# Optimization experiments

Measured on AMD Instinct MI355X. Metric: run time of the kernel, lower is better.

## Reference

```python
import jax, jax.numpy as jnp
import numpy as np

FEATURES = 1024
NUM_HEADS = 16
HEAD_SIZE = FEATURES // NUM_HEADS
B, T = 4, 2048
LN_EPS = 1e-6


def setup_inputs() -> dict:
    key = jax.random.key(0)
    ks = jax.random.split(key, 12)
    C, H, D = FEATURES, NUM_HEADS, HEAD_SIZE
    s_in = 1.0 / np.sqrt(C)
    s_ff = 1.0 / np.sqrt(4 * C)
    return {
        "x": jax.random.normal(ks[0], (B, T, C), jnp.float32),
        # per-head Q/K/V projections (no bias), stacked over heads
        "wq": jax.random.normal(ks[1], (H, C, D), jnp.float32) * s_in,
        "wk": jax.random.normal(ks[2], (H, C, D), jnp.float32) * s_in,
        "wv": jax.random.normal(ks[3], (H, C, D), jnp.float32) * s_in,
        "w_proj": jax.random.normal(ks[4], (C, C), jnp.float32) * s_in,
        "b_proj": jnp.zeros((C,), jnp.float32),
        "w_ff1": jax.random.normal(ks[5], (C, 4 * C), jnp.float32) * s_in,
        "b_ff1": jnp.zeros((4 * C,), jnp.float32),
        "w_ff2": jax.random.normal(ks[6], (4 * C, C), jnp.float32) * s_ff,
        "b_ff2": jnp.zeros((C,), jnp.float32),
        "ln1_scale": jnp.ones((C,), jnp.float32),
        "ln1_bias": jnp.zeros((C,), jnp.float32),
        "ln2_scale": jnp.ones((C,), jnp.float32),
        "ln2_bias": jnp.zeros((C,), jnp.float32),
    }


def _layernorm(x, scale, bias):
    mu = jnp.mean(x, axis=-1, keepdims=True)
    var = jnp.mean(jnp.square(x - mu), axis=-1, keepdims=True)
    return (x - mu) * jax.lax.rsqrt(var + LN_EPS) * scale + bias


def reference(x, wq, wk, wv, w_proj, b_proj, w_ff1, b_ff1, w_ff2, b_ff2,
              ln1_scale, ln1_bias, ln2_scale, ln2_bias):
    Bn, Tn, C = x.shape
    res = x
    xn = _layernorm(x, ln1_scale, ln1_bias)
    # per-head projections, vectorized over heads: [B,H,T,D]
    q = jnp.einsum('btc,hcd->bhtd', xn, wq)
    k = jnp.einsum('btc,hcd->bhtd', xn, wk)
    v = jnp.einsum('btc,hcd->bhtd', xn, wv)
    wei = jnp.einsum('bhtd,bhsd->bhts', q, k)
    tril = jnp.tril(jnp.ones((Tn, Tn), jnp.float32))
    # NOTE: original scales by C**-0.5 (full feature dim, not head_size),
    # and multiplies after masking (-inf * scale stays -inf).
    wei = jnp.where(tril == 0, -jnp.inf, wei) * (C ** -0.5)
    wei = jax.nn.softmax(wei, axis=-1)
    out = jnp.einsum('bhts,bhsd->bhtd', wei, v)
    # concat heads back to [B,T,C]
    out = out.transpose(0, 2, 1, 3).reshape(Bn, Tn, C)
    x = res + out @ w_proj + b_proj
    res = x
    xn = _layernorm(x, ln2_scale, ln2_bias)
    h = jax.nn.relu(xn @ w_ff1 + b_ff1)
    out = res + h @ w_ff2 + b_ff2
    return out
```

## Files before the change

### kernel.cpp

```cpp
#include <hip/hip_runtime.h>

#define Bn 4
#define Tn 2048
#define Cn 1024
#define Hn 16
#define Dn 64
#define Mr (Bn*Tn)

typedef _Float16 half8 __attribute__((ext_vector_type(8)));
typedef _Float16 half4v __attribute__((ext_vector_type(4)));
typedef float f32x4 __attribute__((ext_vector_type(4)));
typedef unsigned u32x4 __attribute__((ext_vector_type(4)));

__device__ __forceinline__ void g2l16(const void* g, void* l) {
  __builtin_amdgcn_global_load_lds((__attribute__((address_space(1))) void*)g,
                                   (__attribute__((address_space(3))) void*)l, 16, 0, 0);
}

__global__ __launch_bounds__(256) void transpose_f32_f16(const float* __restrict__ in,
                                                         _Float16* __restrict__ out,
                                                         int R, int C) {
  __shared__ float tile[32][33];
  const size_t zoff = (size_t)blockIdx.z * R * C;
  in += zoff; out += zoff;
  const int c0 = blockIdx.x * 32, r0 = blockIdx.y * 32;
  const int tx = threadIdx.x, ty = threadIdx.y;
#pragma unroll
  for (int i = 0; i < 4; ++i)
    tile[ty + i*8][tx] = in[(size_t)(r0 + ty + i*8) * C + c0 + tx];
  __syncthreads();
#pragma unroll
  for (int i = 0; i < 4; ++i)
    out[(size_t)(c0 + ty + i*8) * R + r0 + tx] = (_Float16)tile[tx][ty + i*8];
}

__global__ __launch_bounds__(256) void ln_row(const float* __restrict__ x,
                                              const float* __restrict__ g,
                                              const float* __restrict__ bta,
                                              _Float16* __restrict__ out) {
  const int row = blockIdx.x;
  const float4 v = ((const float4*)(x + (size_t)row * Cn))[threadIdx.x];
  float s  = v.x + v.y + v.z + v.w;
  float ss = v.x*v.x + v.y*v.y + v.z*v.z + v.w*v.w;
#pragma unroll
  for (int m = 1; m < 64; m <<= 1) { s += __shfl_xor(s, m); ss += __shfl_xor(ss, m); }
  __shared__ float red[8];
  const int wave = threadIdx.x >> 6, lane = threadIdx.x & 63;
  if (lane == 0) { red[wave] = s; red[4 + wave] = ss; }
  __syncthreads();
  s  = red[0] + red[1] + red[2] + red[3];
  ss = red[4] + red[5] + red[6] + red[7];
  const float mean = s * (1.0f/Cn);
  const float var  = ss * (1.0f/Cn) - mean*mean;
  const float rstd = rsqrtf(var + 1e-6f);
  const int c = threadIdx.x * 4;
  const float4 gg = ((const float4*)g)[threadIdx.x];
  const float4 bb = ((const float4*)bta)[threadIdx.x];
  half4v o;
  o[0] = (_Float16)((v.x - mean) * rstd * gg.x + bb.x);
  o[1] = (_Float16)((v.y - mean) * rstd * gg.y + bb.y);
  o[2] = (_Float16)((v.z - mean) * rstd * gg.z + bb.z);
  o[3] = (_Float16)((v.w - mean) * rstd * gg.w + bb.w);
  *((half4v*)(out + (size_t)row * Cn + c)) = o;
}

enum { EPI_QK = 0, EPI_V = 1, EPI_PROJ = 2, EPI_FF1 = 3, EPI_FF2 = 4 };

template<int EPI>
__global__ __launch_bounds__(256) void gemm_bt(const _Float16* __restrict__ A,
                                               const _Float16* __restrict__ Bt,
                                               void* __restrict__ outp,
                                               const float* __restrict__ bias,
                                               const float* __restrict__ resid,
                                               int M, int N, int K) {
  __shared__ __align__(16) _Float16 As[128*64];
  __shared__ __align__(16) _Float16 Bs[128*64];
  const int tid = threadIdx.x, wave = tid >> 6, lane = tid & 63;
  const int lr = lane & 15, lg = lane >> 4;
  const int brow = blockIdx.y * 128, bcol = blockIdx.x * 128;
  const int wrow = (wave >> 1) * 64, wcol = (wave & 1) * 64;
  f32x4 acc[4][4] = {};

  for (int kt = 0; kt < K; kt += 64) {
#pragma unroll
    for (int i = 0; i < 4; ++i) {
      const int chunk = i*4 + wave;
      const int e = chunk*512 + lane*8;
      const int rr = e >> 6, cc = e & 63;
      g2l16(A  + (size_t)(brow + rr)*K + kt + cc, As + chunk*512);
      g2l16(Bt + (size_t)(bcol + rr)*K + kt + cc, Bs + chunk*512);
    }
    __syncthreads();
#pragma unroll
    for (int kk = 0; kk < 64; kk += 32) {
      half8 af[4], bfr[4];
#pragma unroll
      for (int i = 0; i < 4; ++i) af[i]  = *(const half8*)(As + (wrow + i*16 + lr)*64 + kk + lg*8);
#pragma unroll
      for (int j = 0; j < 4; ++j) bfr[j] = *(const half8*)(Bs + (wcol + j*16 + lr)*64 + kk + lg*8);
#pragma unroll
      for (int i = 0; i < 4; ++i)
#pragma unroll
        for (int j = 0; j < 4; ++j)
          acc[i][j] = __builtin_amdgcn_mfma_f32_16x16x32_f16(af[i], bfr[j], acc[i][j], 0, 0, 0);
    }
    __syncthreads();
  }

  const int r0 = brow + wrow + lg*4;
  const int c0 = bcol + wcol + lr;
#pragma unroll
  for (int i = 0; i < 4; ++i) {
#pragma unroll
    for (int j = 0; j < 4; ++j) {
      const int col = c0 + j*16;
#pragma unroll
      for (int r = 0; r < 4; ++r) {
        const int row = r0 + i*16 + r;
        const float v = acc[i][j][r];
        if constexpr (EPI == EPI_QK) {
          ((_Float16*)outp)[(((size_t)(row >> 11) * Hn + (col >> 6)) * Tn + (row & 2047)) * Dn + (col & 63)] = (_Float16)v;
        } else if constexpr (EPI == EPI_V) {
          ((_Float16*)outp)[(((size_t)(row >> 11) * Hn + (col >> 6)) * Dn + (col & 63)) * Tn + (row & 2047)] = (_Float16)v;
        } else if constexpr (EPI == EPI_PROJ || EPI == EPI_FF2) {
          ((float*)outp)[(size_t)row * N + col] = v + bias[col] + resid[(size_t)row * N + col];
        } else if constexpr (EPI == EPI_FF1) {
          const float t = v + bias[col];
          ((_Float16*)outp)[(size_t)row * N + col] = (_Float16)(t > 0.f ? t : 0.f);
        }
      }
    }
  }
}

__global__ __launch_bounds__(256) void attn_kernel(const _Float16* __restrict__ q,
                                                   const _Float16* __restrict__ k,
                                                   const _Float16* __restrict__ vt,
                                                   _Float16* __restrict__ out) {
  const int qt = (int)(gridDim.x - 1 - blockIdx.x) * 128;
  const int h = blockIdx.y, b = blockIdx.z;
  const int tid = threadIdx.x, wave = tid >> 6, lane = tid & 63;
  const int lr = lane & 15, lg = lane >> 4;
  const size_t bh = (size_t)b * Hn + h;
  const _Float16* qg = q  + bh * (Tn * Dn);
  const _Float16* kg = k  + bh * (Tn * Dn);
  const _Float16* vg = vt + bh * (Dn * Tn);

  __shared__ __align__(16) _Float16 Ks[2][64*64];
  __shared__ __align__(16) _Float16 Vs[2][64*64];

  half8 qf[2][2];
#pragma unroll
  for (int qi = 0; qi < 2; ++qi)
#pragma unroll
    for (int dh = 0; dh < 2; ++dh)
      qf[qi][dh] = *(const half8*)(qg + (size_t)(qt + wave*32 + qi*16 + lr)*Dn + dh*32 + lg*8);

  f32x4 oacc[2][4] = {};
  float mrow[2] = {-__builtin_inff(), -__builtin_inff()};
  float lsum[2] = {0.f, 0.f};

  const int qmax = qt + wave*32 + 31;
  const int nt = (qt + 128) >> 6;

  auto STAGE = [&](int bufi, int t) {
    const int kvt = t * 64;
#pragma unroll
    for (int r = 0; r < 2; ++r) {
      const int g0 = r*256 + wave*64;
      const int g  = g0 + lane;
      const int rr = g >> 3;
      const int cs = (g & 7) ^ (rr & 7);
      g2l16(kg + (size_t)(kvt + rr)*Dn + cs*8, &Ks[bufi][g0*8]);
      g2l16(vg + (size_t)rr*Tn + kvt + cs*8,   &Vs[bufi][g0*8]);
    }
  };

  STAGE(0, 0);
  __syncthreads();

  for (int t = 0; t < nt; ++t) {
    const int kvt = t * 64;
    if (t + 1 < nt) STAGE((t + 1) & 1, t + 1);

    if (kvt <= qmax) {
      const _Float16* KS = Ks[t & 1];
      const _Float16* VS = Vs[t & 1];
      half8 kb[4][2];
#pragma unroll
      for (int f = 0; f < 4; ++f)
#pragma unroll
        for (int dh = 0; dh < 2; ++dh)
          kb[f][dh] = *(const half8*)(KS + (16*f + lr)*64 + (((4*dh + lg) ^ (lr & 7)) * 8));

#pragma unroll
      for (int qi = 0; qi < 2; ++qi) {
        f32x4 sv[4];
#pragma unroll
        for (int f = 0; f < 4; ++f) {
          f32x4 tacc = {0.f, 0.f, 0.f, 0.f};
          tacc = __builtin_amdgcn_mfma_f32_16x16x32_f16(kb[f][0], qf[qi][0], tacc, 0, 0, 0);
          tacc = __builtin_amdgcn_mfma_f32_16x16x32_f16(kb[f][1], qf[qi][1], tacc, 0, 0, 0);
          sv[f] = tacc;
        }
        const int qrow = qt + wave*32 + qi*16 + lr;
#pragma unroll
        for (int f = 0; f < 4; ++f)
#pragma unroll
          for (int r = 0; r < 4; ++r) {
            const int kvv = kvt + 16*f + 4*lg + r;
            sv[f][r] = (kvv > qrow) ? -__builtin_inff() : sv[f][r] * 0.03125f;
          }
        float tm = sv[0][0];
#pragma unroll
        for (int f = 0; f < 4; ++f)
#pragma unroll
          for (int r = 0; r < 4; ++r) tm = fmaxf(tm, sv[f][r]);
        tm = fmaxf(tm, __shfl_xor(tm, 16));
        tm = fmaxf(tm, __shfl_xor(tm, 32));
        const float mn = fmaxf(mrow[qi], tm);
        const float alpha = __expf(mrow[qi] - mn);
        mrow[qi] = mn;
        float ps = 0.f;
#pragma unroll
        for (int f = 0; f < 4; ++f)
#pragma unroll
          for (int r = 0; r < 4; ++r) {
            const float e = __expf(sv[f][r] - mn);
            ps += e;
            sv[f][r] = e;
          }
        ps += __shfl_xor(ps, 16);
        ps += __shfl_xor(ps, 32);
        lsum[qi] = lsum[qi] * alpha + ps;
        unsigned ph[4][2];
#pragma unroll
        for (int f = 0; f < 4; ++f)
#pragma unroll
          for (int m = 0; m < 2; ++m) {
            const unsigned lo = (unsigned)__builtin_bit_cast(unsigned short, (_Float16)sv[f][2*m]);
            const unsigned hi = (unsigned)__builtin_bit_cast(unsigned short, (_Float16)sv[f][2*m + 1]);
            ph[f][m] = lo | (hi << 16);
          }
        float ab[4];
#pragma unroll
        for (int r = 0; r < 4; ++r) ab[r] = __shfl(alpha, 4*lg + r);
#pragma unroll
        for (int df = 0; df < 4; ++df)
#pragma unroll
          for (int r = 0; r < 4; ++r) oacc[qi][df][r] *= ab[r];
        const int s0 = lr + 16*(2*(lg & 1));
        const int s1 = s0 + 16;
        half8 pa[2];
#pragma unroll
        for (int kh = 0; kh < 2; ++kh) {
          u32x4 w = {0u, 0u, 0u, 0u};
#pragma unroll
          for (int fi = 0; fi < 2; ++fi) {
            const unsigned a0 = __shfl(ph[2*kh + fi][0], s0);
            const unsigned a1 = __shfl(ph[2*kh + fi][1], s0);
            const unsigned a2 = __shfl(ph[2*kh + fi][0], s1);
            const unsigned a3 = __shfl(ph[2*kh + fi][1], s1);
            const bool sel = ((lg >> 1) == fi);
            w[0] = sel ? a0 : w[0];
            w[1] = sel ? a1 : w[1];
            w[2] = sel ? a2 : w[2];
            w[3] = sel ? a3 : w[3];
          }
          pa[kh] = __builtin_bit_cast(half8, w);
        }
#pragma unroll
        for (int df = 0; df < 4; ++df) {
          half8 vb0 = *(const half8*)(VS + (16*df + lr)*64 + (((0 + lg) ^ (lr & 7)) * 8));
          half8 vb1 = *(const half8*)(VS + (16*df + lr)*64 + (((4 + lg) ^ (lr & 7)) * 8));
          oacc[qi][df] = __builtin_amdgcn_mfma_f32_16x16x32_f16(pa[0], vb0, oacc[qi][df], 0, 0, 0);
          oacc[qi][df] = __builtin_amdgcn_mfma_f32_16x16x32_f16(pa[1], vb1, oacc[qi][df], 0, 0, 0);
        }
      }
    }
    __syncthreads();
  }

#pragma unroll
  for (int qi = 0; qi < 2; ++qi) {
    const float linv = 1.0f / lsum[qi];
    float lb[4];
#pragma unroll
    for (int r = 0; r < 4; ++r) lb[r] = __shfl(linv, 4*lg + r);
#pragma unroll
    for (int df = 0; df < 4; ++df)
#pragma unroll
      for (int r = 0; r < 4; ++r) {
        const int row = qt + wave*32 + qi*16 + 4*lg + r;
        const int col = h*Dn + df*16 + lr;
        out[((size_t)b*Tn + row)*Cn + col] = (_Float16)(oacc[qi][df][r] * lb[r]);
      }
  }
}

extern "C" void kernel_launch(void* const* d_in, const int* in_sizes, int n_in,
                              void* d_out, int out_size, void* d_ws, size_t ws_size,
                              hipStream_t stream) {
  const float* x      = (const float*)d_in[0];
  const float* wq     = (const float*)d_in[1];
  const float* wk     = (const float*)d_in[2];
  const float* wv     = (const float*)d_in[3];
  const float* w_proj = (const float*)d_in[4];
  const float* b_proj = (const float*)d_in[5];
  const float* b_ff1  = (const float*)d_in[7];
  const float* w_ff1  = (const float*)d_in[6];
  const float* w_ff2  = (const float*)d_in[8];
  const float* b_ff2  = (const float*)d_in[9];
  const float* ln1s   = (const float*)d_in[10];
  const float* ln1b   = (const float*)d_in[11];
  const float* ln2s   = (const float*)d_in[12];
  const float* ln2b   = (const float*)d_in[13];
  float* outp = (float*)d_out;

  char* ws = (char*)d_ws;
  constexpr size_t MB = (size_t)1 << 20;
  _Float16* Wq_t  = (_Float16*)(ws + 0*MB);
  _Float16* Wk_t  = (_Float16*)(ws + 2*MB);
  _Float16* Wv_t  = (_Float16*)(ws + 4*MB);
  _Float16* Wp_t  = (_Float16*)(ws + 6*MB);
  _Float16* Wf1_t = (_Float16*)(ws + 8*MB);
  _Float16* Wf2_t = (_Float16*)(ws + 16*MB);
  _Float16* xn    = (_Float16*)(ws + 24*MB);
  _Float16* attn_o= (_Float16*)(ws + 24*MB);
  _Float16* qbuf  = (_Float16*)(ws + 40*MB);
  _Float16* kbuf  = (_Float16*)(ws + 56*MB);
  _Float16* vtbuf = (_Float16*)(ws + 72*MB);
  _Float16* hbuf  = (_Float16*)(ws + 40*MB);
  float*    x2    = (float*)   (ws + 104*MB);
  _Float16* xn2   = (_Float16*)(ws + 136*MB);

  dim3 tb(32, 8);
  transpose_f32_f16<<<dim3(2, 32, 16), tb, 0, stream>>>(wq, Wq_t, 1024, 64);
  transpose_f32_f16<<<dim3(2, 32, 16), tb, 0, stream>>>(wk, Wk_t, 1024, 64);
  transpose_f32_f16<<<dim3(2, 32, 16), tb, 0, stream>>>(wv, Wv_t, 1024, 64);
  transpose_f32_f16<<<dim3(32, 32, 1), tb, 0, stream>>>(w_proj, Wp_t, 1024, 1024);
  transpose_f32_f16<<<dim3(128, 32, 1), tb, 0, stream>>>(w_ff1, Wf1_t, 1024, 4096);
  transpose_f32_f16<<<dim3(32, 128, 1), tb, 0, stream>>>(w_ff2, Wf2_t, 4096, 1024);

  ln_row<<<Mr, 256, 0, stream>>>(x, ln1s, ln1b, xn);

  gemm_bt<EPI_QK><<<dim3(8, 64), 256, 0, stream>>>(xn, Wq_t, qbuf, nullptr, nullptr, Mr, Cn, Cn);
  gemm_bt<EPI_QK><<<dim3(8, 64), 256, 0, stream>>>(xn, Wk_t, kbuf, nullptr, nullptr, Mr, Cn, Cn);
  gemm_bt<EPI_V ><<<dim3(8, 64), 256, 0, stream>>>(xn, Wv_t, vtbuf, nullptr, nullptr, Mr, Cn, Cn);

  attn_kernel<<<dim3(Tn/128, Hn, Bn), 256, 0, stream>>>(qbuf, kbuf, vtbuf, attn_o);

  gemm_bt<EPI_PROJ><<<dim3(8, 64), 256, 0, stream>>>(attn_o, Wp_t, x2, b_proj, x, Mr, Cn, Cn);

  ln_row<<<Mr, 256, 0, stream>>>(x2, ln2s, ln2b, xn2);

  gemm_bt<EPI_FF1><<<dim3(32, 64), 256, 0, stream>>>(xn2, Wf1_t, hbuf, b_ff1, nullptr, Mr, 4*Cn, Cn);
  gemm_bt<EPI_FF2><<<dim3(8, 64), 256, 0, stream>>>(hbuf, Wf2_t, outp, b_ff2, x2, Mr, Cn, 4*Cn);
}
```

Before: 663.6 us.

## Pair causal query tiles per block to balance attention work and share K/V staging

Each attention block now handles two 128-row query tiles, pi and 15-pi, so every block does about the same amount of causal work. The K/V tiles staged in shared memory are reused by both query tiles. The grid along the sequence axis is halved to 8. The softmax scale is folded into Q in fp16 before the loop, which removes a per-score multiply but adds a small rounding change and doubles accumulator register use, which may lower occupancy.

```diff
diff --git a/kernel.cpp b/kernel.cpp
--- a/kernel.cpp
+++ b/kernel.cpp
@@ -137,7 +137,9 @@
                                                    const _Float16* __restrict__ k,
                                                    const _Float16* __restrict__ vt,
                                                    _Float16* __restrict__ out) {
-  const int qt = (int)(gridDim.x - 1 - blockIdx.x) * 128;
+  const int pi = blockIdx.x;
+  const int qtA = pi * 128;
+  const int qtB = (15 - pi) * 128;
   const int h = blockIdx.y, b = blockIdx.z;
   const int tid = threadIdx.x, wave = tid >> 6, lane = tid & 63;
   const int lr = lane & 15, lg = lane >> 4;
@@ -149,19 +151,25 @@
   __shared__ __align__(16) _Float16 Ks[2][64*64];
   __shared__ __align__(16) _Float16 Vs[2][64*64];
 
-  half8 qf[2][2];
+  const _Float16 qsc = (_Float16)0.03125f;
+  half8 qfA[2][2], qfB[2][2];
 #pragma unroll
   for (int qi = 0; qi < 2; ++qi)
 #pragma unroll
-    for (int dh = 0; dh < 2; ++dh)
-      qf[qi][dh] = *(const half8*)(qg + (size_t)(qt + wave*32 + qi*16 + lr)*Dn + dh*32 + lg*8);
-
-  f32x4 oacc[2][4] = {};
-  float mrow[2] = {-__builtin_inff(), -__builtin_inff()};
-  float lsum[2] = {0.f, 0.f};
-
-  const int qmax = qt + wave*32 + 31;
-  const int nt = (qt + 128) >> 6;
+    for (int dh = 0; dh < 2; ++dh) {
+      half8 a = *(const half8*)(qg + (size_t)(qtA + wave*32 + qi*16 + lr)*Dn + dh*32 + lg*8);
+      half8 c = *(const half8*)(qg + (size_t)(qtB + wave*32 + qi*16 + lr)*Dn + dh*32 + lg*8);
+#pragma unroll
+      for (int j = 0; j < 8; ++j) { a[j] *= qsc; c[j] *= qsc; }
+      qfA[qi][dh] = a; qfB[qi][dh] = c;
+    }
+
+  f32x4 oaccA[2][4] = {}, oaccB[2][4] = {};
+  float mrowA[2] = {-__builtin_inff(), -__builtin_inff()};
+  float mrowB[2] = {-__builtin_inff(), -__builtin_inff()};
+  float lsumA[2] = {0.f, 0.f}, lsumB[2] = {0.f, 0.f};
+
+  const int ntB = (qtB >> 6) + 2;
 
   auto STAGE = [&](int bufi, int t) {
     const int kvt = t * 64;
@@ -176,126 +184,134 @@
     }
   };
 
+  auto COMPUTE = [&](const half8 (&qf)[2][2], f32x4 (&oacc)[2][4],
+                     float* mrow, float* lsum, int qb,
+                     const _Float16* KS, const _Float16* VS, int kvt) {
+    half8 kb[4][2];
+#pragma unroll
+    for (int f = 0; f < 4; ++f)
+#pragma unroll
+      for (int dh = 0; dh < 2; ++dh)
+        kb[f][dh] = *(const half8*)(KS + (16*f + lr)*64 + (((4*dh + lg) ^ (lr & 7)) * 8));
+
+#pragma unroll
+    for (int qi = 0; qi < 2; ++qi) {
+      f32x4 sv[4];
+#pragma unroll
+      for (int f = 0; f < 4; ++f) {
+        f32x4 tacc = {0.f, 0.f, 0.f, 0.f};
+        tacc = __builtin_amdgcn_mfma_f32_16x16x32_f16(kb[f][0], qf[qi][0], tacc, 0, 0, 0);
+        tacc = __builtin_amdgcn_mfma_f32_16x16x32_f16(kb[f][1], qf[qi][1], tacc, 0, 0, 0);
+        sv[f] = tacc;
+      }
+      const int qrow = qb + wave*32 + qi*16 + lr;
+#pragma unroll
+      for (int f = 0; f < 4; ++f)
+#pragma unroll
+        for (int r = 0; r < 4; ++r) {
+          const int kvv = kvt + 16*f + 4*lg + r;
+          sv[f][r] = (kvv > qrow) ? -__builtin_inff() : sv[f][r];
+        }
+      float tm = sv[0][0];
+#pragma unroll
+      for (int f = 0; f < 4; ++f)
+#pragma unroll
+        for (int r = 0; r < 4; ++r) tm = fmaxf(tm, sv[f][r]);
+      tm = fmaxf(tm, __shfl_xor(tm, 16));
+      tm = fmaxf(tm, __shfl_xor(tm, 32));
+      const float mn = fmaxf(mrow[qi], tm);
+      const float alpha = __expf(mrow[qi] - mn);
+      mrow[qi] = mn;
+      float ps = 0.f;
+#pragma unroll
+      for (int f = 0; f < 4; ++f)
+#pragma unroll
+        for (int r = 0; r < 4; ++r) {
+          const float e = __expf(sv[f][r] - mn);
+          ps += e;
+          sv[f][r] = e;
+        }
+      ps += __shfl_xor(ps, 16);
+      ps += __shfl_xor(ps, 32);
+      lsum[qi] = lsum[qi] * alpha + ps;
+      unsigned ph[4][2];
+#pragma unroll
+      for (int f = 0; f < 4; ++f)
+#pragma unroll
+        for (int m = 0; m < 2; ++m) {
+          const unsigned lo = (unsigned)__builtin_bit_cast(unsigned short, (_Float16)sv[f][2*m]);
+          const unsigned hi = (unsigned)__builtin_bit_cast(unsigned short, (_Float16)sv[f][2*m + 1]);
+          ph[f][m] = lo | (hi << 16);
+        }
+      float ab[4];
+#pragma unroll
+      for (int r = 0; r < 4; ++r) ab[r] = __shfl(alpha, 4*lg + r);
+#pragma unroll
+      for (int df = 0; df < 4; ++df)
+#pragma unroll
+        for (int r = 0; r < 4; ++r) oacc[qi][df][r] *= ab[r];
+      const int s0 = lr + 16*(2*(lg & 1));
+      const int s1 = s0 + 16;
+      half8 pa[2];
+#pragma unroll
+      for (int kh = 0; kh < 2; ++kh) {
+        u32x4 w = {0u, 0u, 0u, 0u};
+#pragma unroll
+        for (int fi = 0; fi < 2; ++fi) {
+          const unsigned a0 = __shfl(ph[2*kh + fi][0], s0);
+          const unsigned a1 = __shfl(ph[2*kh + fi][1], s0);
+          const unsigned a2 = __shfl(ph[2*kh + fi][0], s1);
+          const unsigned a3 = __shfl(ph[2*kh + fi][1], s1);
+          const bool sel = ((lg >> 1) == fi);
+          w[0] = sel ? a0 : w[0];
+          w[1] = sel ? a1 : w[1];
+          w[2] = sel ? a2 : w[2];
+          w[3] = sel ? a3 : w[3];
+        }
+        pa[kh] = __builtin_bit_cast(half8, w);
+      }
+#pragma unroll
+      for (int df = 0; df < 4; ++df) {
+        half8 vb0 = *(const half8*)(VS + (16*df + lr)*64 + (((0 + lg) ^ (lr & 7)) * 8));
+        half8 vb1 = *(const half8*)(VS + (16*df + lr)*64 + (((4 + lg) ^ (lr & 7)) * 8));
+        oacc[qi][df] = __builtin_amdgcn_mfma_f32_16x16x32_f16(pa[0], vb0, oacc[qi][df], 0, 0, 0);
+        oacc[qi][df] = __builtin_amdgcn_mfma_f32_16x16x32_f16(pa[1], vb1, oacc[qi][df], 0, 0, 0);
+      }
+    }
+  };
+
   STAGE(0, 0);
   __syncthreads();
 
-  for (int t = 0; t < nt; ++t) {
+  for (int t = 0; t < ntB; ++t) {
     const int kvt = t * 64;
-    if (t + 1 < nt) STAGE((t + 1) & 1, t + 1);
-
-    if (kvt <= qmax) {
-      const _Float16* KS = Ks[t & 1];
-      const _Float16* VS = Vs[t & 1];
-      half8 kb[4][2];
-#pragma unroll
-      for (int f = 0; f < 4; ++f)
-#pragma unroll
-        for (int dh = 0; dh < 2; ++dh)
-          kb[f][dh] = *(const half8*)(KS + (16*f + lr)*64 + (((4*dh + lg) ^ (lr & 7)) * 8));
-
-#pragma unroll
-      for (int qi = 0; qi < 2; ++qi) {
-        f32x4 sv[4];
-#pragma unroll
-        for (int f = 0; f < 4; ++f) {
-          f32x4 tacc = {0.f, 0.f, 0.f, 0.f};
-          tacc = __builtin_amdgcn_mfma_f32_16x16x32_f16(kb[f][0], qf[qi][0], tacc, 0, 0, 0);
-          tacc = __builtin_amdgcn_mfma_f32_16x16x32_f16(kb[f][1], qf[qi][1], tacc, 0, 0, 0);
-          sv[f] = tacc;
-        }
-        const int qrow = qt + wave*32 + qi*16 + lr;
-#pragma unroll
-        for (int f = 0; f < 4; ++f)
-#pragma unroll
-          for (int r = 0; r < 4; ++r) {
-            const int kvv = kvt + 16*f + 4*lg + r;
-            sv[f][r] = (kvv > qrow) ? -__builtin_inff() : sv[f][r] * 0.03125f;
-          }
-        float tm = sv[0][0];
-#pragma unroll
-        for (int f = 0; f < 4; ++f)
-#pragma unroll
-          for (int r = 0; r < 4; ++r) tm = fmaxf(tm, sv[f][r]);
-        tm = fmaxf(tm, __shfl_xor(tm, 16));
-        tm = fmaxf(tm, __shfl_xor(tm, 32));
-        const float mn = fmaxf(mrow[qi], tm);
-        const float alpha = __expf(mrow[qi] - mn);
-        mrow[qi] = mn;
-        float ps = 0.f;
-#pragma unroll
-        for (int f = 0; f < 4; ++f)
-#pragma unroll
-          for (int r = 0; r < 4; ++r) {
-            const float e = __expf(sv[f][r] - mn);
-            ps += e;
-            sv[f][r] = e;
-          }
-        ps += __shfl_xor(ps, 16);
-        ps += __shfl_xor(ps, 32);
-        lsum[qi] = lsum[qi] * alpha + ps;
-        unsigned ph[4][2];
-#pragma unroll
-        for (int f = 0; f < 4; ++f)
-#pragma unroll
-          for (int m = 0; m < 2; ++m) {
-            const unsigned lo = (unsigned)__builtin_bit_cast(unsigned short, (_Float16)sv[f][2*m]);
-            const unsigned hi = (unsigned)__builtin_bit_cast(unsigned short, (_Float16)sv[f][2*m + 1]);
-            ph[f][m] = lo | (hi << 16);
-          }
-        float ab[4];
-#pragma unroll
-        for (int r = 0; r < 4; ++r) ab[r] = __shfl(alpha, 4*lg + r);
-#pragma unroll
-        for (int df = 0; df < 4; ++df)
-#pragma unroll
-          for (int r = 0; r < 4; ++r) oacc[qi][df][r] *= ab[r];
-        const int s0 = lr + 16*(2*(lg & 1));
-        const int s1 = s0 + 16;
-        half8 pa[2];
-#pragma unroll
-        for (int kh = 0; kh < 2; ++kh) {
-          u32x4 w = {0u, 0u, 0u, 0u};
-#pragma unroll
-          for (int fi = 0; fi < 2; ++fi) {
-            const unsigned a0 = __shfl(ph[2*kh + fi][0], s0);
-            const unsigned a1 = __shfl(ph[2*kh + fi][1], s0);
-            const unsigned a2 = __shfl(ph[2*kh + fi][0], s1);
-            const unsigned a3 = __shfl(ph[2*kh + fi][1], s1);
-            const bool sel = ((lg >> 1) == fi);
-            w[0] = sel ? a0 : w[0];
-            w[1] = sel ? a1 : w[1];
-            w[2] = sel ? a2 : w[2];
-            w[3] = sel ? a3 : w[3];
-          }
-          pa[kh] = __builtin_bit_cast(half8, w);
-        }
-#pragma unroll
-        for (int df = 0; df < 4; ++df) {
-          half8 vb0 = *(const half8*)(VS + (16*df + lr)*64 + (((0 + lg) ^ (lr & 7)) * 8));
-          half8 vb1 = *(const half8*)(VS + (16*df + lr)*64 + (((4 + lg) ^ (lr & 7)) * 8));
-          oacc[qi][df] = __builtin_amdgcn_mfma_f32_16x16x32_f16(pa[0], vb0, oacc[qi][df], 0, 0, 0);
-          oacc[qi][df] = __builtin_amdgcn_mfma_f32_16x16x32_f16(pa[1], vb1, oacc[qi][df], 0, 0, 0);
-        }
-      }
-    }
+    if (t + 1 < ntB) STAGE((t + 1) & 1, t + 1);
+    const _Float16* KS = Ks[t & 1];
+    const _Float16* VS = Vs[t & 1];
+    if (kvt <= qtA + wave*32 + 31) COMPUTE(qfA, oaccA, mrowA, lsumA, qtA, KS, VS, kvt);
+    if (kvt <= qtB + wave*32 + 31) COMPUTE(qfB, oaccB, mrowB, lsumB, qtB, KS, VS, kvt);
     __syncthreads();
   }
 
-#pragma unroll
-  for (int qi = 0; qi < 2; ++qi) {
-    const float linv = 1.0f / lsum[qi];
-    float lb[4];
-#pragma unroll
-    for (int r = 0; r < 4; ++r) lb[r] = __shfl(linv, 4*lg + r);
-#pragma unroll
-    for (int df = 0; df < 4; ++df)
-#pragma unroll
-      for (int r = 0; r < 4; ++r) {
-        const int row = qt + wave*32 + qi*16 + 4*lg + r;
-        const int col = h*Dn + df*16 + lr;
-        out[((size_t)b*Tn + row)*Cn + col] = (_Float16)(oacc[qi][df][r] * lb[r]);
-      }
-  }
+  auto EPI = [&](const f32x4 (&oacc)[2][4], const float* lsum, int qb) {
+#pragma unroll
+    for (int qi = 0; qi < 2; ++qi) {
+      const float linv = 1.0f / lsum[qi];
+      float lb[4];
+#pragma unroll
+      for (int r = 0; r < 4; ++r) lb[r] = __shfl(linv, 4*lg + r);
+#pragma unroll
+      for (int df = 0; df < 4; ++df)
+#pragma unroll
+        for (int r = 0; r < 4; ++r) {
+          const int row = qb + wave*32 + qi*16 + 4*lg + r;
+          const int col = h*Dn + df*16 + lr;
+          out[((size_t)b*Tn + row)*Cn + col] = (_Float16)(oacc[qi][df][r] * lb[r]);
+        }
+    }
+  };
+  EPI(oaccA, lsumA, qtA);
+  EPI(oaccB, lsumB, qtB);
 }
 
 extern "C" void kernel_launch(void* const* d_in, const int* in_sizes, int n_in,
@@ -307,8 +323,8 @@
   const float* wv     = (const float*)d_in[3];
   const float* w_proj = (const float*)d_in[4];
   const float* b_proj = (const float*)d_in[5];
+  const float* w_ff1  = (const float*)d_in[6];
   const float* b_ff1  = (const float*)d_in[7];
-  const float* w_ff1  = (const float*)d_in[6];
   const float* w_ff2  = (const float*)d_in[8];
   const float* b_ff2  = (const float*)d_in[9];
   const float* ln1s   = (const float*)d_in[10];
@@ -348,7 +364,7 @@
   gemm_bt<EPI_QK><<<dim3(8, 64), 256, 0, stream>>>(xn, Wk_t, kbuf, nullptr, nullptr, Mr, Cn, Cn);
   gemm_bt<EPI_V ><<<dim3(8, 64), 256, 0, stream>>>(xn, Wv_t, vtbuf, nullptr, nullptr, Mr, Cn, Cn);
 
-  attn_kernel<<<dim3(Tn/128, Hn, Bn), 256, 0, stream>>>(qbuf, kbuf, vtbuf, attn_o);
+  attn_kernel<<<dim3(8, Hn, Bn), 256, 0, stream>>>(qbuf, kbuf, vtbuf, attn_o);
 
   gemm_bt<EPI_PROJ><<<dim3(8, 64), 256, 0, stream>>>(attn_o, Wp_t, x2, b_proj, x, Mr, Cn, Cn);
 
```

Result: faster. 620.6 us (-6.5%).
